# Performance work log

Measured on AMD Instinct MI355X. Metric: run time of the kernel, lower is better.

Reference implementation:

```python
import jax, jax.numpy as jnp
import numpy as np

N, E, C = 50000, 800000, 128
NEG_SLOPE = 0.01

def leaky(v):
    return jnp.where(v >= 0, v, NEG_SLOPE * v)

def setup_inputs() -> dict:
    key = jax.random.key(0)
    ks = jax.random.split(key, 16)
    s = lambda *sh: 1.0 / np.sqrt(sh[0])
    return {
        "x": jax.random.normal(ks[0], (N, C), dtype=jnp.float32),
        "pos": jax.random.normal(ks[1], (N, 3), dtype=jnp.float32),
        "edge_index": jax.random.randint(ks[2], (2, E), 0, N, dtype=jnp.int64),
        # mlp_h: Linear(C,C) -> LeakyReLU -> Linear(C,3) -> Tanh
        "h_w1": jax.random.uniform(ks[3], (C, C), jnp.float32, -s(C), s(C)),
        "h_b1": jax.random.uniform(ks[4], (C,), jnp.float32, -s(C), s(C)),
        "h_w2": jax.random.uniform(ks[5], (C, 3), jnp.float32, -s(C), s(C)),
        "h_b2": jax.random.uniform(ks[6], (3,), jnp.float32, -s(C), s(C)),
        # mlp_f: Linear(C+3, C) -> LeakyReLU
        "f_w": jax.random.uniform(ks[7], (C + 3, C), jnp.float32, -s(C + 3), s(C + 3)),
        "f_b": jax.random.uniform(ks[8], (C,), jnp.float32, -s(C + 3), s(C + 3)),
        # mlp_g: Linear(C,C) -> LeakyReLU -> Linear(C,C)
        "g_w1": jax.random.uniform(ks[9], (C, C), jnp.float32, -s(C), s(C)),
        "g_b1": jax.random.uniform(ks[10], (C,), jnp.float32, -s(C), s(C)),
        "g_w2": jax.random.uniform(ks[11], (C, C), jnp.float32, -s(C), s(C)),
        "g_b2": jax.random.uniform(ks[12], (C,), jnp.float32, -s(C), s(C)),
    }

def reference(x, pos, edge_index, h_w1, h_b1, h_w2, h_b2, f_w, f_b,
              g_w1, g_b1, g_w2, g_b2):
    src = edge_index[0]  # j (source)
    dst = edge_index[1]  # i (target)
    # delta_i = mlp_h(x_i): [N, 3]
    delta = jnp.tanh(leaky(x @ h_w1 + h_b1) @ h_w2 + h_b2)
    # edge message: mlp_f(cat([pos_j - pos_i + delta_i, x_j]))  -> [E, C]
    rel = pos[src] - pos[dst] + delta[dst]            # [E, 3]
    msg_in = jnp.concatenate([rel, x[src]], axis=-1)  # [E, C+3]
    e = leaky(msg_in @ f_w + f_b)                     # [E, C]
    # sum-aggregate messages at target nodes
    aggr = jax.ops.segment_sum(e, dst, num_segments=N)  # [N, C]
    # out = mlp_g(aggr) + x
    out = leaky(aggr @ g_w1 + g_b1) @ g_w2 + g_b2 + x
    return out
```

## Files before the change

kernel.cpp:

```cpp
#include <hip/hip_runtime.h>
#include <hip/hip_bf16.h>
#include <math.h>


typedef __attribute__((ext_vector_type(8))) short bf16x8;
typedef __attribute__((ext_vector_type(4))) float f32x4;

#define LEAKY(v) ((v) >= 0.0f ? (v) : 0.01f * (v))

#define KMAX 512
#define S3_BATCH 4096
#define HB 256
#define AGG_CAP 16384

static __device__ __forceinline__ unsigned short f2bf(float f) {
    unsigned u = __float_as_uint(f);
    u = (u + 0x7fffu + ((u >> 16) & 1u)) >> 16;
    return (unsigned short)u;
}

union ABu { unsigned short u[8]; bf16x8 v; };

static __device__ __forceinline__ bf16x8 cvt8(const float* __restrict__ p) {
    ABu r;
    const float4 v0 = *(const float4*)p;
    const float4 v1 = *(const float4*)(p + 4);
    r.u[0] = f2bf(v0.x); r.u[1] = f2bf(v0.y); r.u[2] = f2bf(v0.z); r.u[3] = f2bf(v0.w);
    r.u[4] = f2bf(v1.x); r.u[5] = f2bf(v1.y); r.u[6] = f2bf(v1.z); r.u[7] = f2bf(v1.w);
    return r.v;
}

static __device__ __forceinline__ bf16x8 zero_ab() {
    ABu r;
    #pragma unroll
    for (int i = 0; i < 8; ++i) r.u[i] = 0;
    return r.v;
}

static __device__ __forceinline__ void proc8(
    const uint4 v, const float* __restrict__ qd, float* __restrict__ acc)
{
    const float f0 = __uint_as_float((v.x & 0xffffu) << 16);
    const float f1 = __uint_as_float(v.x & 0xffff0000u);
    const float f2 = __uint_as_float((v.y & 0xffffu) << 16);
    const float f3 = __uint_as_float(v.y & 0xffff0000u);
    const float f4 = __uint_as_float((v.z & 0xffffu) << 16);
    const float f5 = __uint_as_float(v.z & 0xffff0000u);
    const float f6 = __uint_as_float((v.w & 0xffffu) << 16);
    const float f7 = __uint_as_float(v.w & 0xffff0000u);
    const float z0 = f0 + qd[0], z1 = f1 + qd[1];
    const float z2 = f2 + qd[2], z3 = f3 + qd[3];
    const float z4 = f4 + qd[4], z5 = f5 + qd[5];
    const float z6 = f6 + qd[6], z7 = f7 + qd[7];
    acc[0] += fmaxf(z0, 0.01f * z0);
    acc[1] += fmaxf(z1, 0.01f * z1);
    acc[2] += fmaxf(z2, 0.01f * z2);
    acc[3] += fmaxf(z3, 0.01f * z3);
    acc[4] += fmaxf(z4, 0.01f * z4);
    acc[5] += fmaxf(z5, 0.01f * z5);
    acc[6] += fmaxf(z6, 0.01f * z6);
    acc[7] += fmaxf(z7, 0.01f * z7);
}

static __device__ __forceinline__ void stage_weight(
    const unsigned short* __restrict__ src, unsigned short (*dst)[136], int tid)
{
    #pragma unroll
    for (int it = 0; it < 8; ++it) {
        const int c   = it * 256 + tid;
        const int row = c >> 4;
        const int col = (c & 15) * 8;
        *(uint4*)&dst[row][col] = *(const uint4*)(src + row * 128 + col);
    }
}

__global__ __launch_bounds__(128) void prep_weights(
    const float* __restrict__ h_w1, const float* __restrict__ f_w,
    const float* __restrict__ g_w1, const float* __restrict__ g_w2,
    unsigned short* __restrict__ Wht, unsigned short* __restrict__ Wft,
    unsigned short* __restrict__ G1t, unsigned short* __restrict__ G2t,
    int* __restrict__ bincnt, int* __restrict__ done)
{
    const int j = blockIdx.x;
    const int k = threadIdx.x;
    if (j == 0) {
        for (int i = k; i < KMAX; i += 128) bincnt[i] = 0;
        if (k == 0) *done = 0;
    }
    Wht[j * 128 + k] = f2bf(h_w1[(size_t)k * 128 + j]);
    Wft[j * 128 + k] = f2bf(f_w[(size_t)(3 + k) * 128 + j]);
    G1t[j * 128 + k] = f2bf(g_w1[(size_t)k * 128 + j]);
    G2t[j * 128 + k] = f2bf(g_w2[(size_t)k * 128 + j]);
}

__global__ __launch_bounds__(256) void fused_pre(
    const float* __restrict__ x, const float* __restrict__ pos,
    const unsigned short* __restrict__ Wht, const float* __restrict__ h_b1,
    const float* __restrict__ h_w2, const float* __restrict__ h_b2,
    const unsigned short* __restrict__ Wft, const float* __restrict__ f_b,
    const float* __restrict__ fw3,
    float* __restrict__ deltap, unsigned short* __restrict__ Zb,
    const int* __restrict__ ei, int* __restrict__ bincnt,
    int* __restrict__ binstart, int* __restrict__ cursors,
    int* __restrict__ done, int E, int K, int N)
{
    __shared__ __align__(16) unsigned char smem[34816 + 4096];
    __shared__ int lastflag;

    const int tid = threadIdx.x;

    if (blockIdx.x < HB) {
        int* h = (int*)smem;
        int* s = (int*)(smem + 2048);
        for (int k = tid; k < K; k += 256) h[k] = 0;
        __syncthreads();
        if ((E & 3) == 0) {
            const int E4 = E >> 2;
            const uint4* d4 = (const uint4*)(ei + (size_t)E);
            for (int i = blockIdx.x * 256 + tid; i < E4; i += HB * 256) {
                const uint4 v = d4[i];
                atomicAdd(&h[v.x >> 7], 1);
                atomicAdd(&h[v.y >> 7], 1);
                atomicAdd(&h[v.z >> 7], 1);
                atomicAdd(&h[v.w >> 7], 1);
            }
        } else {
            for (int e = blockIdx.x * 256 + tid; e < E; e += HB * 256)
                atomicAdd(&h[ei[(size_t)E + e] >> 7], 1);
        }
        __syncthreads();
        for (int k = tid; k < K; k += 256) {
            const int v = h[k];
            if (v) atomicAdd(&bincnt[k], v);
        }
        __threadfence();
        __syncthreads();
        if (tid == 0) lastflag = (atomicAdd(done, 1) == HB - 1) ? 1 : 0;
        __syncthreads();
        if (!lastflag) return;

        const int i0 = tid * 2;
        const int c0 = (i0 < K)     ? atomicAdd(&bincnt[i0], 0)     : 0;
        const int c1 = (i0 + 1 < K) ? atomicAdd(&bincnt[i0 + 1], 0) : 0;
        s[tid] = c0 + c1;
        __syncthreads();
        for (int d = 1; d < 256; d <<= 1) {
            const int t = (tid >= d) ? s[tid - d] : 0;
            __syncthreads();
            s[tid] += t;
            __syncthreads();
        }
        const int ex = s[tid] - (c0 + c1);
        if (i0 < K)     { binstart[i0]     = ex;      cursors[i0]     = ex; }
        if (i0 + 1 < K) { binstart[i0 + 1] = ex + c0; cursors[i0 + 1] = ex + c0; }
        if (tid == 0) binstart[K] = E;
        return;
    }

    unsigned short (*Ws)[136] = (unsigned short (*)[136])smem;
    float (*cb)[8] = (float (*)[8])(smem + 34816);

    const int lane = tid & 63;
    const int wave = tid >> 6;
    const int quad = lane >> 4;
    const int l16  = lane & 15;
    const int row0 = (blockIdx.x - HB) * 64 + wave * 16;

    if (tid < 128) {
        cb[tid][0] = h_b1[tid];
        cb[tid][1] = f_b[tid];
        cb[tid][2] = h_w2[tid * 3 + 0];
        cb[tid][3] = h_w2[tid * 3 + 1];
        cb[tid][4] = h_w2[tid * 3 + 2];
        cb[tid][5] = fw3[tid];
        cb[tid][6] = fw3[128 + tid];
        cb[tid][7] = fw3[256 + tid];
    }
    stage_weight(Wht, Ws, tid);

    bf16x8 a[4];
    {
        const int row = row0 + l16;
        if (row < N) {
            const float* xp = x + (size_t)row * 128 + quad * 8;
            #pragma unroll
            for (int kc = 0; kc < 4; ++kc) a[kc] = cvt8(xp + kc * 32);
        } else {
            #pragma unroll
            for (int kc = 0; kc < 4; ++kc) a[kc] = zero_ab();
        }
    }

    float px[4], py[4], pz[4];
    #pragma unroll
    for (int reg = 0; reg < 4; ++reg) {
        const int grow = row0 + quad * 4 + reg;
        const int gr = (grow < N) ? grow : 0;
        px[reg] = pos[(size_t)gr * 3 + 0];
        py[reg] = pos[(size_t)gr * 3 + 1];
        pz[reg] = pos[(size_t)gr * 3 + 2];
    }
    __syncthreads();

    f32x4 acch[8];
    #pragma unroll
    for (int nt = 0; nt < 8; ++nt) acch[nt] = (f32x4){0.f, 0.f, 0.f, 0.f};
    #pragma unroll
    for (int nt = 0; nt < 8; ++nt) {
        const unsigned short* wp = &Ws[nt * 16 + l16][quad * 8];
        #pragma unroll
        for (int kc = 0; kc < 4; ++kc) {
            const bf16x8 b = *(const bf16x8*)(wp + kc * 32);
            acch[nt] = __builtin_amdgcn_mfma_f32_16x16x32_bf16(a[kc], b, acch[nt], 0, 0, 0);
        }
    }

    __syncthreads();
    stage_weight(Wft, Ws, tid);
    __syncthreads();

    f32x4 accf[8];
    #pragma unroll
    for (int nt = 0; nt < 8; ++nt) accf[nt] = (f32x4){0.f, 0.f, 0.f, 0.f};
    #pragma unroll
    for (int nt = 0; nt < 8; ++nt) {
        const unsigned short* wp = &Ws[nt * 16 + l16][quad * 8];
        #pragma unroll
        for (int kc = 0; kc < 4; ++kc) {
            const bf16x8 b = *(const bf16x8*)(wp + kc * 32);
            accf[nt] = __builtin_amdgcn_mfma_f32_16x16x32_bf16(a[kc], b, accf[nt], 0, 0, 0);
        }
    }

    float p[4][3];
    #pragma unroll
    for (int r = 0; r < 4; ++r) { p[r][0] = 0.f; p[r][1] = 0.f; p[r][2] = 0.f; }

    #pragma unroll
    for (int nt = 0; nt < 8; ++nt) {
        const int col = nt * 16 + l16;
        const float b1  = cb[col][0];
        const float fb  = cb[col][1];
        const float w20 = cb[col][2];
        const float w21 = cb[col][3];
        const float w22 = cb[col][4];
        const float wxc = cb[col][5];
        const float wyc = cb[col][6];
        const float wzc = cb[col][7];
        #pragma unroll
        for (int reg = 0; reg < 4; ++reg) {
            const int grow = row0 + quad * 4 + reg;
            float h = acch[nt][reg] + b1;
            h = LEAKY(h);
            p[reg][0] += h * w20;
            p[reg][1] += h * w21;
            p[reg][2] += h * w22;
            if (grow < N) {
                const float z = accf[nt][reg] + fb
                              + px[reg] * wxc + py[reg] * wyc + pz[reg] * wzc;
                Zb[(size_t)grow * 128 + col] = f2bf(z);
            }
        }
    }

    #pragma unroll
    for (int reg = 0; reg < 4; ++reg)
        #pragma unroll
        for (int c = 0; c < 3; ++c) {
            float v = p[reg][c];
            v += __shfl_down(v, 8);
            v += __shfl_down(v, 4);
            v += __shfl_down(v, 2);
            v += __shfl_down(v, 1);
            p[reg][c] = v;
        }

    if (l16 == 0) {
        #pragma unroll
        for (int reg = 0; reg < 4; ++reg) {
            const int grow = row0 + quad * 4 + reg;
            if (grow < N) {
                deltap[(size_t)grow * 3 + 0] = tanhf(p[reg][0] + h_b2[0]) - px[reg];
                deltap[(size_t)grow * 3 + 1] = tanhf(p[reg][1] + h_b2[1]) - py[reg];
                deltap[(size_t)grow * 3 + 2] = tanhf(p[reg][2] + h_b2[2]) - pz[reg];
            }
        }
    }
}

__global__ __launch_bounds__(512) void binsort(
    const int* __restrict__ ei, int* __restrict__ cursors,
    unsigned int* __restrict__ binned, int E, int K)
{
    __shared__ int h[KMAX];
    __shared__ int hE[KMAX];
    __shared__ int cur[KMAX];
    __shared__ int gbase[KMAX];
    __shared__ int s[512];
    __shared__ unsigned int stage[S3_BATCH];
    __shared__ unsigned short binid[S3_BATCH];

    const int tid = threadIdx.x;
    const int e0  = blockIdx.x * S3_BATCH;
    const int m   = min(S3_BATCH, E - e0);

    for (int k = tid; k < K; k += 512) h[k] = 0;
    __syncthreads();

    #pragma unroll
    for (int j = 0; j < S3_BATCH / 512; ++j) {
        const int i = j * 512 + tid;
        if (i < m) atomicAdd(&h[ei[(size_t)E + e0 + i] >> 7], 1);
    }
    __syncthreads();

    const int c = (tid < K) ? h[tid] : 0;
    s[tid] = c;
    __syncthreads();
    for (int d = 1; d < 512; d <<= 1) {
        const int t = (tid >= d) ? s[tid - d] : 0;
        __syncthreads();
        s[tid] += t;
        __syncthreads();
    }
    if (tid < K) {
        const int ex = s[tid] - c;
        hE[tid]  = ex;
        cur[tid] = ex;
        gbase[tid] = c ? atomicAdd(&cursors[tid], c) : 0;
    }
    __syncthreads();

    #pragma unroll
    for (int j = 0; j < S3_BATCH / 512; ++j) {
        const int i = j * 512 + tid;
        if (i < m) {
            const int src = ei[e0 + i];
            const int dst = ei[(size_t)E + e0 + i];
            const int k = dst >> 7;
            const int p = atomicAdd(&cur[k], 1);
            stage[p] = (unsigned int)src | ((unsigned int)(dst & 127) << 16);
            binid[p] = (unsigned short)k;
        }
    }
    __syncthreads();

    #pragma unroll
    for (int j = 0; j < S3_BATCH / 512; ++j) {
        const int i = j * 512 + tid;
        if (i < m) {
            const int k = binid[i];
            binned[(size_t)gbase[k] + (i - hE[k])] = stage[i];
        }
    }
}

__global__ __launch_bounds__(512) void bin_csr_aggregate(
    const unsigned int* __restrict__ binned, const int* __restrict__ binstart,
    const float* __restrict__ deltap,
    const unsigned short* __restrict__ Zb,
    const float* __restrict__ fw3,
    unsigned short* __restrict__ srcs_g,
    unsigned short* __restrict__ Ab,
    int N)
{
    __shared__ int h[64];
    __shared__ int s[64];
    __shared__ int cur[64];
    __shared__ unsigned short sl[AGG_CAP];

    const int tid  = threadIdx.x;
    const int bin  = blockIdx.x >> 1;
    const int half = blockIdx.x & 1;
    const int s0   = binstart[bin];
    const int s1   = binstart[bin + 1];
    const int len  = s1 - s0;

    if (tid < 64) h[tid] = 0;
    __syncthreads();

    for (int i = tid; i < len; i += 512) {
        const int dl16 = binned[(size_t)s0 + i] >> 16;
        if ((dl16 >> 6) == half) atomicAdd(&h[dl16 & 63], 1);
    }
    __syncthreads();

    if (tid < 64) s[tid] = h[tid];
    __syncthreads();
    for (int d = 1; d < 64; d <<= 1) {
        int t = 0;
        if (tid < 64 && tid >= d) t = s[tid - d];
        __syncthreads();
        if (tid < 64) s[tid] += t;
        __syncthreads();
    }
    if (tid < 64) cur[tid] = s[tid] - h[tid];
    __syncthreads();

    const int own   = s[63];
    const bool fits = (own <= AGG_CAP);
    const int gb    = half ? (s1 - own) : s0;

    for (int i = tid; i < len; i += 512) {
        const unsigned int r = binned[(size_t)s0 + i];
        const int dl16 = r >> 16;
        if ((dl16 >> 6) == half) {
            const int p = atomicAdd(&cur[dl16 & 63], 1);
            if (fits) sl[p] = (unsigned short)(r & 0xffffu);
            else      srcs_g[(size_t)gb + p] = (unsigned short)(r & 0xffffu);
        }
    }
    __threadfence_block();
    __syncthreads();

    const int lane    = tid & 63;
    const int wv      = tid >> 6;
    const int quarter = lane >> 4;
    const int cl      = (lane & 15) * 8;
    const int d0      = bin * 128 + half * 64;

    for (int dl = wv; dl < 64; dl += 8) {
        const int d = d0 + dl;
        if (d >= N) continue;

        const int len_d = h[dl];
        const int start = s[dl] - h[dl];

        const float q0 = deltap[(size_t)d * 3 + 0];
        const float q1 = deltap[(size_t)d * 3 + 1];
        const float q2 = deltap[(size_t)d * 3 + 2];

        float qd[8];
        #pragma unroll
        for (int j = 0; j < 8; ++j)
            qd[j] = q0 * fw3[cl + j] + q1 * fw3[128 + cl + j] + q2 * fw3[256 + cl + j];

        float acc[8] = {0.f, 0.f, 0.f, 0.f, 0.f, 0.f, 0.f, 0.f};

        for (int chunk = 0; chunk < len_d; chunk += 64) {
            const int m = min(64, len_d - chunk);
            int idx = 0;
            if (lane < m)
                idx = fits ? (int)sl[start + chunk + lane]
                           : (int)srcs_g[(size_t)gb + start + chunk + lane];

            int t = 0;
            for (; t + 8 <= m; t += 8) {
                const int sA = __shfl(idx, t + quarter);
                const int sB = __shfl(idx, t + 4 + quarter);
                const uint4 yA = *(const uint4*)(Zb + (size_t)sA * 128 + cl);
                const uint4 yB = *(const uint4*)(Zb + (size_t)sB * 128 + cl);
                proc8(yA, qd, acc);
                proc8(yB, qd, acc);
            }
            if (t + 4 <= m) {
                const int sA = __shfl(idx, t + quarter);
                const uint4 yA = *(const uint4*)(Zb + (size_t)sA * 128 + cl);
                proc8(yA, qd, acc);
                t += 4;
            }
            if (t < m) {
                const int e = t + quarter;
                const int sA = __shfl(idx, e);
                if (e < m) {
                    const uint4 yA = *(const uint4*)(Zb + (size_t)sA * 128 + cl);
                    proc8(yA, qd, acc);
                }
            }
        }

        #pragma unroll
        for (int j = 0; j < 8; ++j) {
            acc[j] += __shfl_xor(acc[j], 16);
            acc[j] += __shfl_xor(acc[j], 32);
        }
        if (quarter == 0) {
            ABu o;
            #pragma unroll
            for (int j = 0; j < 8; ++j) o.u[j] = f2bf(acc[j]);
            *(bf16x8*)(Ab + (size_t)d * 128 + cl) = o.v;
        }
    }
}

__global__ __launch_bounds__(256) void gemm_g(
    const unsigned short* __restrict__ Ab,
    const unsigned short* __restrict__ G1t, const float* __restrict__ g_b1,
    const unsigned short* __restrict__ G2t, const float* __restrict__ g_b2,
    const float* __restrict__ x,
    float* __restrict__ out, int N)
{
    __shared__ unsigned short Ws[128][136];
    __shared__ unsigned short Ts[64][136];

    const int tid  = threadIdx.x;
    const int lane = tid & 63;
    const int wave = tid >> 6;
    const int quad = lane >> 4;
    const int l16  = lane & 15;
    const int row0 = blockIdx.x * 64 + wave * 16;

    stage_weight(G1t, Ws, tid);

    bf16x8 a[4];
    {
        const int row = row0 + l16;
        if (row < N) {
            const unsigned short* ap = Ab + (size_t)row * 128 + quad * 8;
            #pragma unroll
            for (int kc = 0; kc < 4; ++kc) a[kc] = *(const bf16x8*)(ap + kc * 32);
        } else {
            #pragma unroll
            for (int kc = 0; kc < 4; ++kc) a[kc] = zero_ab();
        }
    }
    __syncthreads();

    f32x4 acc[8];
    #pragma unroll
    for (int nt = 0; nt < 8; ++nt) acc[nt] = (f32x4){0.f, 0.f, 0.f, 0.f};
    #pragma unroll
    for (int nt = 0; nt < 8; ++nt) {
        const unsigned short* wp = &Ws[nt * 16 + l16][quad * 8];
        #pragma unroll
        for (int kc = 0; kc < 4; ++kc) {
            const bf16x8 b = *(const bf16x8*)(wp + kc * 32);
            acc[nt] = __builtin_amdgcn_mfma_f32_16x16x32_bf16(a[kc], b, acc[nt], 0, 0, 0);
        }
    }

    #pragma unroll
    for (int nt = 0; nt < 8; ++nt) {
        const int col = nt * 16 + l16;
        const float b1 = g_b1[col];
        #pragma unroll
        for (int reg = 0; reg < 4; ++reg) {
            float t = acc[nt][reg] + b1;
            t = LEAKY(t);
            Ts[wave * 16 + quad * 4 + reg][col] = f2bf(t);
        }
    }
    __syncthreads();
    stage_weight(G2t, Ws, tid);
    __syncthreads();

    bf16x8 a2[4];
    {
        const unsigned short* tp = &Ts[wave * 16 + l16][quad * 8];
        #pragma unroll
        for (int kc = 0; kc < 4; ++kc) a2[kc] = *(const bf16x8*)(tp + kc * 32);
    }

    f32x4 acc2[8];
    #pragma unroll
    for (int nt = 0; nt < 8; ++nt) acc2[nt] = (f32x4){0.f, 0.f, 0.f, 0.f};
    #pragma unroll
    for (int nt = 0; nt < 8; ++nt) {
        const unsigned short* wp = &Ws[nt * 16 + l16][quad * 8];
        #pragma unroll
        for (int kc = 0; kc < 4; ++kc) {
            const bf16x8 b = *(const bf16x8*)(wp + kc * 32);
            acc2[nt] = __builtin_amdgcn_mfma_f32_16x16x32_bf16(a2[kc], b, acc2[nt], 0, 0, 0);
        }
    }

    #pragma unroll
    for (int nt = 0; nt < 8; ++nt) {
        const int col = nt * 16 + l16;
        const float b2 = g_b2[col];
        #pragma unroll
        for (int reg = 0; reg < 4; ++reg) {
            const int grow = row0 + quad * 4 + reg;
            if (grow < N)
                out[(size_t)grow * 128 + col] =
                    acc2[nt][reg] + b2 + x[(size_t)grow * 128 + col];
        }
    }
}

extern "C" void kernel_launch(void* const* d_in, const int* in_sizes, int n_in,
                              void* d_out, int out_size, void* d_ws, size_t ws_size,
                              hipStream_t stream) {
    const float* x    = (const float*)d_in[0];
    const float* pos  = (const float*)d_in[1];
    const int*   ei   = (const int*)d_in[2];
    const float* h_w1 = (const float*)d_in[3];
    const float* h_b1 = (const float*)d_in[4];
    const float* h_w2 = (const float*)d_in[5];
    const float* h_b2 = (const float*)d_in[6];
    const float* f_w  = (const float*)d_in[7];
    const float* f_b  = (const float*)d_in[8];
    const float* g_w1 = (const float*)d_in[9];
    const float* g_b1 = (const float*)d_in[10];
    const float* g_w2 = (const float*)d_in[11];
    const float* g_b2 = (const float*)d_in[12];
    float* out = (float*)d_out;

    const int N = in_sizes[0] / 128;
    const int E = in_sizes[2] / 2;
    const int K = (N + 127) >> 7;

    float* deltap         = (float*)d_ws;
    unsigned short* Zb    = (unsigned short*)(deltap + (size_t)N * 3);
    int* bincnt           = (int*)(Zb + (size_t)N * 128);
    int* binstart         = bincnt + KMAX;
    int* cursors          = binstart + (KMAX + 1);
    int* done             = cursors + KMAX;
    unsigned int* binned  = (unsigned int*)(done + 1);
    unsigned short* srcs  = (unsigned short*)(binned + E);
    unsigned short* Wht   = srcs + (((size_t)E + 1) & ~(size_t)1);
    unsigned short* Wft   = Wht + 128 * 128;
    unsigned short* G1t   = Wft + 128 * 128;
    unsigned short* G2t   = G1t + 128 * 128;
    unsigned short* Ab    = G2t + 128 * 128;

    const int tile_blocks = (N + 63) / 64;
    const int sort_blocks = (E + S3_BATCH - 1) / S3_BATCH;

    prep_weights<<<128, 128, 0, stream>>>(h_w1, f_w, g_w1, g_w2, Wht, Wft, G1t, G2t,
                                          bincnt, done);

    fused_pre<<<HB + tile_blocks, 256, 0, stream>>>(
        x, pos, Wht, h_b1, h_w2, h_b2, Wft, f_b, f_w,
        deltap, Zb, ei, bincnt, binstart, cursors, done, E, K, N);

    binsort<<<sort_blocks, 512, 0, stream>>>(ei, cursors, binned, E, K);

    bin_csr_aggregate<<<K * 2, 512, 0, stream>>>(binned, binstart, deltap, Zb, f_w,
                                                 srcs, Ab, N);

    gemm_g<<<tile_blocks, 256, 0, stream>>>(Ab, G1t, g_b1, G2t, g_b2, x, out, N);
}
```

Before: 230.7 us.

## Use wave-shuffle scans and vectorized edge loads in binsort, simplify gather loop

Replaces the barrier-heavy shared-memory Hillis-Steele scans in binsort and bin_csr_aggregate with wavefront shuffle scans plus a small cross-wave combine. It also loads destination and source indices as uint4 vectors once, keeps them in registers, and packs the bin id into the staged word so the separate binid array and a second read of the edges are dropped. The gather loop in aggregation becomes a single unroll-by-4 loop. The trade-off is extra register use and a packed encoding that assumes source ids fit in 16 bits.

```diff
diff --git a/kernel.cpp b/kernel.cpp
--- a/kernel.cpp
+++ b/kernel.cpp
@@ -62,6 +62,16 @@
     acc[7] += fmaxf(z7, 0.01f * z7);
 }
 
+static __device__ __forceinline__ int wave_incl_scan(int v) {
+    const int lane = threadIdx.x & 63;
+    #pragma unroll
+    for (int d = 1; d < 64; d <<= 1) {
+        const int t = __shfl_up(v, d);
+        if (lane >= d) v += t;
+    }
+    return v;
+}
+
 static __device__ __forceinline__ void stage_weight(
     const unsigned short* __restrict__ src, unsigned short (*dst)[136], int tid)
 {
@@ -296,38 +306,86 @@
     __shared__ int hE[KMAX];
     __shared__ int cur[KMAX];
     __shared__ int gbase[KMAX];
-    __shared__ int s[512];
+    __shared__ int wsum[8];
     __shared__ unsigned int stage[S3_BATCH];
-    __shared__ unsigned short binid[S3_BATCH];
 
     const int tid = threadIdx.x;
     const int e0  = blockIdx.x * S3_BATCH;
     const int m   = min(S3_BATCH, E - e0);
+    const bool vec = (m == S3_BATCH) && ((E & 3) == 0);
 
     for (int k = tid; k < K; k += 512) h[k] = 0;
     __syncthreads();
 
-    #pragma unroll
-    for (int j = 0; j < S3_BATCH / 512; ++j) {
-        const int i = j * 512 + tid;
-        if (i < m) atomicAdd(&h[ei[(size_t)E + e0 + i] >> 7], 1);
-    }
-    __syncthreads();
-
-    const int c = (tid < K) ? h[tid] : 0;
-    s[tid] = c;
-    __syncthreads();
-    for (int d = 1; d < 512; d <<= 1) {
-        const int t = (tid >= d) ? s[tid - d] : 0;
+    unsigned int dsts[8];
+    if (vec) {
+        const uint4* dv = (const uint4*)(ei + (size_t)E + e0);
+        const uint4 a0 = dv[tid];
+        const uint4 a1 = dv[tid + 512];
+        dsts[0] = a0.x; dsts[1] = a0.y; dsts[2] = a0.z; dsts[3] = a0.w;
+        dsts[4] = a1.x; dsts[5] = a1.y; dsts[6] = a1.z; dsts[7] = a1.w;
+        #pragma unroll
+        for (int j = 0; j < 8; ++j) atomicAdd(&h[dsts[j] >> 7], 1);
+    } else {
+        #pragma unroll
+        for (int j = 0; j < 8; ++j) {
+            const int i = (j < 4) ? (4 * tid + j) : (S3_BATCH / 2 + 4 * tid + j - 4);
+            dsts[j] = 0;
+            if (i < m) {
+                dsts[j] = (unsigned int)ei[(size_t)E + e0 + i];
+                atomicAdd(&h[dsts[j] >> 7], 1);
+            }
+        }
+    }
+    __syncthreads();
+
+    {
+        const int c = (tid < K) ? h[tid] : 0;
+        int sc = wave_incl_scan(c);
+        if ((tid & 63) == 63) wsum[tid >> 6] = sc;
         __syncthreads();
-        s[tid] += t;
+        if (tid < 64) {
+            int w = (tid < 8) ? wsum[tid] : 0;
+            #pragma unroll
+            for (int d = 1; d < 8; d <<= 1) {
+                const int t = __shfl_up(w, d);
+                if (tid >= d) w += t;
+            }
+            if (tid < 8) wsum[tid] = w;
+        }
         __syncthreads();
-    }
-    if (tid < K) {
-        const int ex = s[tid] - c;
-        hE[tid]  = ex;
-        cur[tid] = ex;
-        gbase[tid] = c ? atomicAdd(&cursors[tid], c) : 0;
+        if (tid >= 64) sc += wsum[(tid >> 6) - 1];
+        if (tid < K) {
+            const int ex = sc - c;
+            hE[tid]  = ex;
+            cur[tid] = ex;
+            gbase[tid] = c ? atomicAdd(&cursors[tid], c) : 0;
+        }
+    }
+    __syncthreads();
+
+    if (vec) {
+        const uint4* sv = (const uint4*)(ei + (size_t)e0);
+        const uint4 b0 = sv[tid];
+        const uint4 b1 = sv[tid + 512];
+        unsigned int srcs[8];
+        srcs[0] = b0.x; srcs[1] = b0.y; srcs[2] = b0.z; srcs[3] = b0.w;
+        srcs[4] = b1.x; srcs[5] = b1.y; srcs[6] = b1.z; srcs[7] = b1.w;
+        #pragma unroll
+        for (int j = 0; j < 8; ++j) {
+            const int p = atomicAdd(&cur[dsts[j] >> 7], 1);
+            stage[p] = srcs[j] | (dsts[j] << 16);
+        }
+    } else {
+        #pragma unroll
+        for (int j = 0; j < 8; ++j) {
+            const int i = (j < 4) ? (4 * tid + j) : (S3_BATCH / 2 + 4 * tid + j - 4);
+            if (i < m) {
+                const unsigned int src = (unsigned int)ei[(size_t)e0 + i];
+                const int p = atomicAdd(&cur[dsts[j] >> 7], 1);
+                stage[p] = src | (dsts[j] << 16);
+            }
+        }
     }
     __syncthreads();
 
@@ -335,22 +393,9 @@
     for (int j = 0; j < S3_BATCH / 512; ++j) {
         const int i = j * 512 + tid;
         if (i < m) {
-            const int src = ei[e0 + i];
-            const int dst = ei[(size_t)E + e0 + i];
-            const int k = dst >> 7;
-            const int p = atomicAdd(&cur[k], 1);
-            stage[p] = (unsigned int)src | ((unsigned int)(dst & 127) << 16);
-            binid[p] = (unsigned short)k;
-        }
-    }
-    __syncthreads();
-
-    #pragma unroll
-    for (int j = 0; j < S3_BATCH / 512; ++j) {
-        const int i = j * 512 + tid;
-        if (i < m) {
-            const int k = binid[i];
-            binned[(size_t)gbase[k] + (i - hE[k])] = stage[i];
+            const unsigned int r = stage[i];
+            const int k = r >> 23;
+            binned[(size_t)gbase[k] + (i - hE[k])] = r & 0x007FFFFFu;
         }
     }
 }
@@ -385,16 +430,12 @@
     }
     __syncthreads();
 
-    if (tid < 64) s[tid] = h[tid];
-    __syncthreads();
-    for (int d = 1; d < 64; d <<= 1) {
-        int t = 0;
-        if (tid < 64 && tid >= d) t = s[tid - d];
-        __syncthreads();
-        if (tid < 64) s[tid] += t;
-        __syncthreads();
-    }
-    if (tid < 64) cur[tid] = s[tid] - h[tid];
+    if (tid < 64) {
+        const int hv = h[tid];
+        const int sc = wave_incl_scan(hv);
+        s[tid]   = sc;
+        cur[tid] = sc - hv;
+    }
     __syncthreads();
 
     const int own   = s[63];
@@ -445,26 +486,18 @@
                            : (int)srcs_g[(size_t)gb + start + chunk + lane];
 
             int t = 0;
-            for (; t + 8 <= m; t += 8) {
-                const int sA = __shfl(idx, t + quarter);
-                const int sB = __shfl(idx, t + 4 + quarter);
-                const uint4 yA = *(const uint4*)(Zb + (size_t)sA * 128 + cl);
-                const uint4 yB = *(const uint4*)(Zb + (size_t)sB * 128 + cl);
-                proc8(yA, qd, acc);
-                proc8(yB, qd, acc);
-            }
-            if (t + 4 <= m) {
-                const int sA = __shfl(idx, t + quarter);
-                const uint4 yA = *(const uint4*)(Zb + (size_t)sA * 128 + cl);
-                proc8(yA, qd, acc);
-                t += 4;
+            #pragma unroll 4
+            for (; t + 4 <= m; t += 4) {
+                const int sidx = __shfl(idx, t + quarter);
+                const uint4 y = *(const uint4*)(Zb + (size_t)sidx * 128 + cl);
+                proc8(y, qd, acc);
             }
             if (t < m) {
                 const int e = t + quarter;
-                const int sA = __shfl(idx, e);
+                const int sidx = __shfl(idx, e);
                 if (e < m) {
-                    const uint4 yA = *(const uint4*)(Zb + (size_t)sA * 128 + cl);
-                    proc8(yA, qd, acc);
+                    const uint4 y = *(const uint4*)(Zb + (size_t)sidx * 128 + cl);
+                    proc8(y, qd, acc);
                 }
             }
         }
```

After: 216.4 us, median of 2. 1.07x faster.
